# Kernel optimization log

Hardware: AMD Instinct MI355X
Metric: run time of the kernel (lower is better)

The kernel has to match this reference:

```python
import jax, jax.numpy as jnp
import numpy as np

G, N, F_IN, H, C = 128, 512, 128, 128, 10
LAMB = 1.0
NEG_SLOPE = 0.2
P_EDGE = 32.0 / N  # avg degree ~32


def setup_inputs() -> dict:
    key = jax.random.key(0)
    ks = jax.random.split(key, 12)
    x = jax.random.normal(ks[0], (G, N, F_IN), dtype=jnp.float32)
    # symmetric 0/1 adjacency without self loops (per-graph dense block)
    a = (jax.random.uniform(ks[1], (G, N, N)) < P_EDGE).astype(jnp.float32)
    adj = jnp.maximum(a, jnp.swapaxes(a, 1, 2)) * (1.0 - jnp.eye(N, dtype=jnp.float32))

    def lin(k, fi, fo):
        return (jax.random.normal(k, (fi, fo), dtype=jnp.float32) / np.float32(np.sqrt(fi)))

    return {
        "x": x, "adj": adj,
        "W1": lin(ks[2], F_IN, H), "b1": jnp.zeros((H,), jnp.float32),
        "W2": lin(ks[3], H, H), "b2": jnp.zeros((H,), jnp.float32),
        "W3": lin(ks[4], H, H), "b3": jnp.zeros((H,), jnp.float32),
        "att1_s": 0.1 * jax.random.normal(ks[5], (H,), dtype=jnp.float32),
        "att1_d": 0.1 * jax.random.normal(ks[6], (H,), dtype=jnp.float32),
        "att2_s": 0.1 * jax.random.normal(ks[7], (H,), dtype=jnp.float32),
        "att2_d": 0.1 * jax.random.normal(ks[8], (H,), dtype=jnp.float32),
        "Wl1": lin(ks[9], 2 * H, H), "bl1": jnp.zeros((H,), jnp.float32),
        "Wl2": lin(ks[10], H, H // 2), "bl2": jnp.zeros((H // 2,), jnp.float32),
        "Wl3": lin(ks[11], H // 2, C), "bl3": jnp.zeros((C,), jnp.float32),
    }


def gcn(x, adj, W, b):
    # GCNConv: D^{-1/2} (A + I) D^{-1/2} X W + b  (self-loop weight 1, edge weights in adj)
    deg = adj.sum(-1) + 1.0                              # [G, n]
    dinv = jax.lax.rsqrt(deg)
    xw = x @ W                                           # [G, n, H]
    agg = jnp.einsum('gij,gjf->gif', adj, dinv[..., None] * xw)
    return dinv[..., None] * agg + (dinv * dinv)[..., None] * xw + b


def info_score(x, adj):
    # HGP-SL node information score: row-wise L1 norm of (I - D^{-1} A) X
    deg = jnp.maximum(adj.sum(-1), 1.0)
    agg = jnp.einsum('gij,gjf->gif', adj, x) / deg[..., None]
    return jnp.sum(jnp.abs(x - agg), axis=-1)            # [G, n]


def hgpsl_pool(x, adj, att_s, att_d, k):
    # top-k node selection by information score, then structure learning:
    # dense (sample=False) path: e_ij = leaky_relu(att.[x_i||x_j]) + lamb*A_ij, softmax over j
    s = info_score(x, adj)
    _, idx = jax.lax.top_k(s, k)                         # [G, k]
    xk = jnp.take_along_axis(x, idx[..., None], axis=1)  # [G, k, H]
    g = jnp.arange(x.shape[0])[:, None, None]
    ak = adj[g, idx[:, :, None], idx[:, None, :]]        # induced adjacency [G, k, k]
    e = jax.nn.leaky_relu((xk @ att_s)[:, :, None] + (xk @ att_d)[:, None, :], NEG_SLOPE)
    attn = jax.nn.softmax(e + LAMB * ak, axis=-1)        # new learned edge weights
    return xk, attn


def readout(x):
    # gmp || gap over nodes
    return jnp.concatenate([x.max(axis=1), x.mean(axis=1)], axis=-1)


def reference(x, adj, W1, b1, W2, b2, W3, b3, att1_s, att1_d, att2_s, att2_d,
              Wl1, bl1, Wl2, bl2, Wl3, bl3):
    h = jax.nn.relu(gcn(x, adj, W1, b1))
    h, a1 = hgpsl_pool(h, adj, att1_s, att1_d, N // 2)
    x1 = readout(h)
    h = jax.nn.relu(gcn(h, a1, W2, b2))
    h, a2 = hgpsl_pool(h, a1, att2_s, att2_d, N // 4)
    x2 = readout(h)
    h = jax.nn.relu(gcn(h, a2, W3, b3))
    x3 = readout(h)
    z = jax.nn.relu(x1) + jax.nn.relu(x2) + jax.nn.relu(x3)
    z = jax.nn.relu(z @ Wl1 + bl1)
    z = jax.nn.relu(z @ Wl2 + bl2)
    return jax.nn.softmax(z @ Wl3 + bl3, axis=-1)
```

## Files before the change

### kernel.cpp

```cpp
#include <hip/hip_runtime.h>

#define Gg   128
#define N1   512
#define FH   128
#define K1   256
#define K2   128

typedef unsigned short ush;
typedef __bf16 bf16x8 __attribute__((ext_vector_type(8)));
typedef float  floatx4 __attribute__((ext_vector_type(4)));

__device__ inline float wredsum(float v) {
#pragma unroll
    for (int o = 32; o; o >>= 1) v += __shfl_xor(v, o, 64);
    return v;
}
__device__ inline float wredmax(float v) {
#pragma unroll
    for (int o = 32; o; o >>= 1) v = fmaxf(v, __shfl_xor(v, o, 64));
    return v;
}
__device__ inline ush bf_rne(float x) {
    unsigned u = __float_as_uint(x);
    return (ush)((u + 0x7fffu + ((u >> 16) & 1u)) >> 16);
}
__device__ inline float bf2f(ush u) { return __uint_as_float((unsigned)u << 16); }
__device__ inline void split3(float v, ush& h, ush& m, ush& l) {
    h = bf_rne(v);
    float r1 = v - bf2f(h);
    m = bf_rne(r1);
    l = bf_rne(r1 - bf2f(m));
}
__device__ __forceinline__ bf16x8 expand_bits(unsigned word, int quad) {
    unsigned byte = (word >> (quad * 8)) & 0xffu;
    unsigned au[4] __attribute__((aligned(16)));
    au[0] = ((byte & 1u)   ? 0x3F80u : 0u) | ((byte & 2u)   ? 0x3F800000u : 0u);
    au[1] = ((byte & 4u)   ? 0x3F80u : 0u) | ((byte & 8u)   ? 0x3F800000u : 0u);
    au[2] = ((byte & 16u)  ? 0x3F80u : 0u) | ((byte & 32u)  ? 0x3F800000u : 0u);
    au[3] = ((byte & 64u)  ? 0x3F80u : 0u) | ((byte & 128u) ? 0x3F800000u : 0u);
    return *(const bf16x8*)au;
}

__global__ __launch_bounds__(256) void k_prep(const float* __restrict__ adj,
        float* __restrict__ dinv_gcn, float* __restrict__ dinv_info,
        unsigned* __restrict__ adjbits) {
    int wave = threadIdx.x >> 6, lane = threadIdx.x & 63;
    long long row = (long long)blockIdx.x * 4 + wave;
    const float* ar = adj + row * N1;
    float s = 0.f;
    unsigned myw = 0;
#pragma unroll
    for (int c = 0; c < 8; ++c) {
        float v = ar[c * 64 + lane];
        s += v;
        unsigned long long mk = __ballot(v != 0.0f);
        unsigned lo = (unsigned)mk, hi = (unsigned)(mk >> 32);
        if ((lane >> 1) == c) myw = (lane & 1) ? hi : lo;
    }
    if (lane < 16) adjbits[row * 16 + lane] = myw;
    s = wredsum(s);
    if (lane == 0) {
        dinv_gcn[row]  = rsqrtf(s + 1.0f);
        dinv_info[row] = 1.0f / fmaxf(s, 1.0f);
    }
}

__global__ __launch_bounds__(256) void k_gemm_rw(const float* __restrict__ A,
        const float* __restrict__ W, float* __restrict__ C,
        const float* __restrict__ rs) {
    __shared__ float Al[64][68];
    __shared__ float Wl[64][132];
    long long row0 = (long long)blockIdx.x * 64;
    int tid = threadIdx.x, tr = tid >> 4, tc = tid & 15;
    float acc[4][8] = {};
    for (int ch = 0; ch < 2; ++ch) {
        for (int p = tid; p < 1024; p += 256) {
            int r = p >> 4, c4 = p & 15;
            *(float4*)&Al[r][c4 * 4] = *(const float4*)(A + (row0 + r) * 128 + ch * 64 + c4 * 4);
        }
        for (int p = tid; p < 2048; p += 256) {
            int r = p >> 5, c4 = p & 31;
            *(float4*)&Wl[r][c4 * 4] = *(const float4*)(W + (ch * 64 + r) * 128 + c4 * 4);
        }
        __syncthreads();
        for (int k = 0; k < 64; ++k) {
            float4 w0 = *(const float4*)&Wl[k][tc * 8];
            float4 w1 = *(const float4*)&Wl[k][tc * 8 + 4];
            float w[8] = {w0.x, w0.y, w0.z, w0.w, w1.x, w1.y, w1.z, w1.w};
#pragma unroll
            for (int i = 0; i < 4; ++i) {
                float a = Al[tr * 4 + i][k];
#pragma unroll
                for (int j = 0; j < 8; ++j) acc[i][j] = fmaf(a, w[j], acc[i][j]);
            }
        }
        __syncthreads();
    }
#pragma unroll
    for (int i = 0; i < 4; ++i) {
        long long r = row0 + tr * 4 + i;
        float sc = rs ? rs[r] : 1.0f;
        *(float4*)(C + r * 128 + tc * 8)     = make_float4(sc * acc[i][0], sc * acc[i][1], sc * acc[i][2], sc * acc[i][3]);
        *(float4*)(C + r * 128 + tc * 8 + 4) = make_float4(sc * acc[i][4], sc * acc[i][5], sc * acc[i][6], sc * acc[i][7]);
    }
}

template<int KD>
__global__ __launch_bounds__(256) void k_tsplit(const float* __restrict__ feat,
        ush* __restrict__ Thi, ush* __restrict__ Tmid, ush* __restrict__ Tlo) {
    __shared__ float tile[64 * 65];
    int b = blockIdx.x;
    int cb = b & 1;
    long long row0 = (long long)(b >> 1) * 64;
    int g = (int)(row0 / KD);
    int rk0 = (int)(row0 % KD);
    int t = threadIdx.x;
    {
        int r0 = t >> 4, c4 = t & 15;
#pragma unroll
        for (int i = 0; i < 4; ++i) {
            int r = r0 + i * 16;
            float4 v = *(const float4*)(feat + (row0 + r) * 128 + cb * 64 + c4 * 4);
            tile[r * 65 + c4 * 4 + 0] = v.x;
            tile[r * 65 + c4 * 4 + 1] = v.y;
            tile[r * 65 + c4 * 4 + 2] = v.z;
            tile[r * 65 + c4 * 4 + 3] = v.w;
        }
    }
    __syncthreads();
    int tf = t >> 2, chunk = t & 3;
    ush hbuf[16] __attribute__((aligned(16)));
    ush mbuf[16] __attribute__((aligned(16)));
    ush lbuf[16] __attribute__((aligned(16)));
#pragma unroll
    for (int i = 0; i < 16; ++i) {
        int m = chunk * 16 + i;
        split3(tile[m * 65 + tf], hbuf[i], mbuf[i], lbuf[i]);
    }
    long long obase = ((long long)g * 128 + cb * 64 + tf) * KD + rk0 + chunk * 16;
    *(uint4*)(Thi + obase)      = *(const uint4*)&hbuf[0];
    *(uint4*)(Thi + obase + 8)  = *(const uint4*)&hbuf[8];
    *(uint4*)(Tmid + obase)     = *(const uint4*)&mbuf[0];
    *(uint4*)(Tmid + obase + 8) = *(const uint4*)&mbuf[8];
    *(uint4*)(Tlo + obase)      = *(const uint4*)&lbuf[0];
    *(uint4*)(Tlo + obase + 8)  = *(const uint4*)&lbuf[8];
}

template<int EPI>
__global__ __launch_bounds__(256) void k_aggbT(const unsigned* __restrict__ adjbits,
        const ush* __restrict__ Ahi, const ush* __restrict__ Amid, const ush* __restrict__ Alo,
        const float* __restrict__ dvec, const float* __restrict__ hx,
        const float* __restrict__ bias, float* __restrict__ outH, float* __restrict__ outS) {
    __shared__ unsigned bitsL[128 * 17];
    __shared__ float sred[2][128];
    int b = blockIdx.x;
    int g  = (b & 7) + ((b >> 5) << 3);
    int ib = (b >> 3) & 3;
    int tid = threadIdx.x;
    int w = tid >> 6, lane = tid & 63;
    int wm = w >> 1, wn = w & 1;
    int ln = lane & 15, quad = lane >> 4;
    {
        int r = tid >> 1, w8 = (tid & 1) * 8;
        const unsigned* src = adjbits + ((long long)(g * 512 + ib * 128 + r)) * 16 + w8;
        uint4 v0 = *(const uint4*)src;
        uint4 v1 = *(const uint4*)(src + 4);
        unsigned* dst = &bitsL[r * 17 + w8];
        dst[0] = v0.x; dst[1] = v0.y; dst[2] = v0.z; dst[3] = v0.w;
        dst[4] = v1.x; dst[5] = v1.y; dst[6] = v1.z; dst[7] = v1.w;
    }
    __syncthreads();
    floatx4 acc[4][4];
#pragma unroll
    for (int i = 0; i < 4; ++i)
#pragma unroll
        for (int j = 0; j < 4; ++j) { floatx4 z = {0.f, 0.f, 0.f, 0.f}; acc[i][j] = z; }

    long long aoff[4];
#pragma unroll
    for (int tm = 0; tm < 4; ++tm)
        aoff[tm] = ((long long)g * 128 + wm * 64 + tm * 16 + ln) * 512 + quad * 8;
    int boffL[4];
#pragma unroll
    for (int tn = 0; tn < 4; ++tn)
        boffL[tn] = (wn * 64 + tn * 16 + ln) * 17;

#pragma unroll 2
    for (int kt = 0; kt < 16; ++kt) {
        int kk = kt * 32;
        bf16x8 ah[4], am[4], al[4];
#pragma unroll
        for (int tm = 0; tm < 4; ++tm) {
            ah[tm] = *(const bf16x8*)(Ahi  + aoff[tm] + kk);
            am[tm] = *(const bf16x8*)(Amid + aoff[tm] + kk);
            al[tm] = *(const bf16x8*)(Alo  + aoff[tm] + kk);
        }
#pragma unroll
        for (int tn = 0; tn < 4; ++tn) {
            bf16x8 bb = expand_bits(bitsL[boffL[tn] + kt], quad);
#pragma unroll
            for (int tm = 0; tm < 4; ++tm) {
                acc[tm][tn] = __builtin_amdgcn_mfma_f32_16x16x32_bf16(ah[tm], bb, acc[tm][tn], 0, 0, 0);
                acc[tm][tn] = __builtin_amdgcn_mfma_f32_16x16x32_bf16(am[tm], bb, acc[tm][tn], 0, 0, 0);
                acc[tm][tn] = __builtin_amdgcn_mfma_f32_16x16x32_bf16(al[tm], bb, acc[tm][tn], 0, 0, 0);
            }
        }
    }
    if (EPI == 0) {
#pragma unroll
        for (int tn = 0; tn < 4; ++tn) {
            long long grow = (long long)g * 512 + ib * 128 + wn * 64 + tn * 16 + ln;
            float di = dvec[grow];
#pragma unroll
            for (int tm = 0; tm < 4; ++tm) {
                int f0 = wm * 64 + tm * 16 + quad * 4;
                float4 hv = *(const float4*)(hx + grow * 128 + f0);
                float4 bv = *(const float4*)(bias + f0);
                float4 o;
                o.x = fmaxf(fmaf(di, acc[tm][tn][0] + hv.x, bv.x), 0.f);
                o.y = fmaxf(fmaf(di, acc[tm][tn][1] + hv.y, bv.y), 0.f);
                o.z = fmaxf(fmaf(di, acc[tm][tn][2] + hv.z, bv.z), 0.f);
                o.w = fmaxf(fmaf(di, acc[tm][tn][3] + hv.w, bv.w), 0.f);
                *(float4*)(outH + grow * 128 + f0) = o;
            }
        }
    } else {
#pragma unroll
        for (int tn = 0; tn < 4; ++tn) {
            int il = wn * 64 + tn * 16 + ln;
            long long grow = (long long)g * 512 + ib * 128 + il;
            float di = dvec[grow];
            float p = 0.f;
#pragma unroll
            for (int tm = 0; tm < 4; ++tm) {
                int f0 = wm * 64 + tm * 16 + quad * 4;
                float4 hv = *(const float4*)(hx + grow * 128 + f0);
                p += fabsf(hv.x - acc[tm][tn][0] * di) + fabsf(hv.y - acc[tm][tn][1] * di)
                   + fabsf(hv.z - acc[tm][tn][2] * di) + fabsf(hv.w - acc[tm][tn][3] * di);
            }
            p += __shfl_xor(p, 16); p += __shfl_xor(p, 32);
            if (quad == 0) sred[wm][il] = p;
        }
        __syncthreads();
        if (tid < 128)
            outS[(long long)g * 512 + ib * 128 + tid] = sred[0][tid] + sred[1][tid];
    }
}

template<int KD, int TM, int EPI>
__global__ __launch_bounds__(256) void k_aggsT(
        const ush* __restrict__ Fhi, const ush* __restrict__ Fmid, const ush* __restrict__ Flo,
        const ush* __restrict__ Phi, const ush* __restrict__ Pmid, const ush* __restrict__ Plo,
        const float* __restrict__ dvec, const float* __restrict__ hx,
        const float* __restrict__ bias, float* __restrict__ outH, float* __restrict__ outS) {
    __shared__ float sred[2][128];
    constexpr int FB = TM * 32;
    constexpr int bpgF = 128 / FB;
    constexpr int bpgI = KD / 128;
    constexpr int BPG = bpgF * bpgI;
    int b = blockIdx.x;
    int g   = (b & 7) + ((b / (8 * BPG)) << 3);
    int sub = (b >> 3) % BPG;
    int fb = sub / bpgI, ib2 = sub % bpgI;
    int tid = threadIdx.x;
    int w = tid >> 6, lane = tid & 63;
    int wm = w >> 1, wn = w & 1;
    int ln = lane & 15, quad = lane >> 4;
    floatx4 acc[TM][4];
#pragma unroll
    for (int i = 0; i < TM; ++i)
#pragma unroll
        for (int j = 0; j < 4; ++j) { floatx4 z = {0.f, 0.f, 0.f, 0.f}; acc[i][j] = z; }

    long long aoff[TM], boff[4];
#pragma unroll
    for (int tm = 0; tm < TM; ++tm)
        aoff[tm] = ((long long)g * 128 + fb * FB + wm * (FB / 2) + tm * 16 + ln) * KD + quad * 8;
#pragma unroll
    for (int tn = 0; tn < 4; ++tn)
        boff[tn] = ((long long)g * KD + ib2 * 128 + wn * 64 + tn * 16 + ln) * KD + quad * 8;

#pragma unroll 2
    for (int kt = 0; kt < KD / 32; ++kt) {
        int kk = kt * 32;
        bf16x8 ah[TM], am[TM], al[TM];
#pragma unroll
        for (int tm = 0; tm < TM; ++tm) {
            ah[tm] = *(const bf16x8*)(Fhi  + aoff[tm] + kk);
            am[tm] = *(const bf16x8*)(Fmid + aoff[tm] + kk);
            al[tm] = *(const bf16x8*)(Flo  + aoff[tm] + kk);
        }
#pragma unroll
        for (int tn = 0; tn < 4; ++tn) {
            bf16x8 bh = *(const bf16x8*)(Phi  + boff[tn] + kk);
            bf16x8 bm = *(const bf16x8*)(Pmid + boff[tn] + kk);
            bf16x8 bl = *(const bf16x8*)(Plo  + boff[tn] + kk);
#pragma unroll
            for (int tm = 0; tm < TM; ++tm) {
                floatx4 a = acc[tm][tn];
                a = __builtin_amdgcn_mfma_f32_16x16x32_bf16(ah[tm], bh, a, 0, 0, 0);
                a = __builtin_amdgcn_mfma_f32_16x16x32_bf16(ah[tm], bm, a, 0, 0, 0);
                a = __builtin_amdgcn_mfma_f32_16x16x32_bf16(am[tm], bh, a, 0, 0, 0);
                a = __builtin_amdgcn_mfma_f32_16x16x32_bf16(ah[tm], bl, a, 0, 0, 0);
                a = __builtin_amdgcn_mfma_f32_16x16x32_bf16(al[tm], bh, a, 0, 0, 0);
                a = __builtin_amdgcn_mfma_f32_16x16x32_bf16(am[tm], bm, a, 0, 0, 0);
                acc[tm][tn] = a;
            }
        }
    }
    if (EPI == 0) {
#pragma unroll
        for (int tn = 0; tn < 4; ++tn) {
            long long grow = (long long)g * KD + ib2 * 128 + wn * 64 + tn * 16 + ln;
            float di = dvec[grow];
#pragma unroll
            for (int tm = 0; tm < TM; ++tm) {
                int f0 = fb * FB + wm * (FB / 2) + tm * 16 + quad * 4;
                float4 hv = *(const float4*)(hx + grow * 128 + f0);
                float4 bv = *(const float4*)(bias + f0);
                float4 o;
                o.x = fmaxf(fmaf(di, acc[tm][tn][0] + hv.x, bv.x), 0.f);
                o.y = fmaxf(fmaf(di, acc[tm][tn][1] + hv.y, bv.y), 0.f);
                o.z = fmaxf(fmaf(di, acc[tm][tn][2] + hv.z, bv.z), 0.f);
                o.w = fmaxf(fmaf(di, acc[tm][tn][3] + hv.w, bv.w), 0.f);
                *(float4*)(outH + grow * 128 + f0) = o;
            }
        }
    } else {
#pragma unroll
        for (int tn = 0; tn < 4; ++tn) {
            int il = wn * 64 + tn * 16 + ln;
            long long grow = (long long)g * KD + ib2 * 128 + il;
            float di = dvec[grow];
            float p = 0.f;
#pragma unroll
            for (int tm = 0; tm < TM; ++tm) {
                int f0 = fb * FB + wm * (FB / 2) + tm * 16 + quad * 4;
                float4 hv = *(const float4*)(hx + grow * 128 + f0);
                p += fabsf(hv.x - acc[tm][tn][0] * di) + fabsf(hv.y - acc[tm][tn][1] * di)
                   + fabsf(hv.z - acc[tm][tn][2] * di) + fabsf(hv.w - acc[tm][tn][3] * di);
            }
            p += __shfl_xor(p, 16); p += __shfl_xor(p, 32);
            if (quad == 0) sred[wm][il] = p;
        }
        __syncthreads();
        if (tid < 128)
            outS[(long long)g * KD + ib2 * 128 + tid] = sred[0][tid] + sred[1][tid];
    }
}

template<int NT, int KSEL>
__global__ __launch_bounds__(256) void k_topk(const float* __restrict__ s, int* __restrict__ idx) {
    __shared__ unsigned long long keys[NT];
    int g = blockIdx.x;
    const float* sg = s + g * NT;
    for (int t = threadIdx.x; t < NT; t += 256) {
        unsigned int b = __float_as_uint(sg[t]);
        unsigned int ord = (b & 0x80000000u) ? ~b : (b | 0x80000000u);
        keys[t] = ((unsigned long long)(~ord) << 32) | (unsigned int)t;
    }
    __syncthreads();
    for (int k = 2; k <= NT; k <<= 1) {
        for (int j = k >> 1; j > 0; j >>= 1) {
            for (int i = threadIdx.x; i < NT; i += 256) {
                int l = i ^ j;
                if (l > i) {
                    bool dir = ((i & k) == 0);
                    unsigned long long a = keys[i], b2 = keys[l];
                    bool sw = dir ? (a > b2) : (a < b2);
                    if (sw) { keys[i] = b2; keys[l] = a; }
                }
            }
            __syncthreads();
        }
    }
    for (int t = threadIdx.x; t < KSEL; t += 256)
        idx[g * KSEL + t] = (int)(keys[t] & 0xffffffffu);
}

template<int KK>
__global__ __launch_bounds__(256) void k_gather(const float* __restrict__ h, int srcN,
        const int* __restrict__ idx, const float* __restrict__ atts, const float* __restrict__ attd,
        float* __restrict__ xk, float* __restrict__ as_, float* __restrict__ ad_) {
    int wave = threadIdx.x >> 6, lane = threadIdx.x & 63;
    int r = blockIdx.x * 4 + wave;
    int g = r / KK;
    int j = idx[r];
    float2 v = *(const float2*)(h + ((long long)g * srcN + j) * 128 + lane * 2);
    *(float2*)(xk + (long long)r * 128 + lane * 2) = v;
    float2 sv = *(const float2*)(atts + lane * 2);
    float2 dv = *(const float2*)(attd + lane * 2);
    float ps = v.x * sv.x + v.y * sv.y;
    float pd = v.x * dv.x + v.y * dv.y;
    ps = wredsum(ps); pd = wredsum(pd);
    if (lane == 0) { as_[r] = ps; ad_[r] = pd; }
}

__global__ __launch_bounds__(256) void k_attn1b(const unsigned* __restrict__ adjbits,
        const int* __restrict__ idx, const float* __restrict__ as_, const float* __restrict__ ad_,
        float* __restrict__ a1, ush* __restrict__ Ahi, ush* __restrict__ Amid, ush* __restrict__ Alo,
        float* __restrict__ dgo, float* __restrict__ dio) {
    __shared__ int   idxL[K1];
    __shared__ float adL[K1];
    __shared__ unsigned bitsW[4][20];
    __shared__ float rowL[4][K1];
    int g = blockIdx.x / (K1 / 4);
    int wave = threadIdx.x >> 6, lane = threadIdx.x & 63;
    int i = (blockIdx.x % (K1 / 4)) * 4 + wave;
    for (int t = threadIdx.x; t < K1; t += 256) { idxL[t] = idx[g * K1 + t]; adL[t] = ad_[g * K1 + t]; }
    __syncthreads();
    int ri = idxL[i];
    if (lane < 4) {
        uint4 v = *(const uint4*)(adjbits + ((long long)(g * 512 + ri)) * 16 + lane * 4);
        bitsW[wave][lane * 4 + 0] = v.x; bitsW[wave][lane * 4 + 1] = v.y;
        bitsW[wave][lane * 4 + 2] = v.z; bitsW[wave][lane * 4 + 3] = v.w;
    }
    __syncthreads();
    float asi = as_[g * K1 + i];
    float vals[4];
    float m = -1e30f;
#pragma unroll
    for (int e = 0; e < 4; ++e) {
        int j = e * 64 + lane;
        float x = asi + adL[j];
        x = (x >= 0.f) ? x : 0.2f * x;
        int jj = idxL[j];
        unsigned bit = (bitsW[wave][jj >> 5] >> (jj & 31)) & 1u;
        x += (float)bit;
        vals[e] = x; m = fmaxf(m, x);
    }
    m = wredmax(m);
    float S = 0.f;
#pragma unroll
    for (int e = 0; e < 4; ++e) { vals[e] = expf(vals[e] - m); S += vals[e]; }
    S = wredsum(S);
    float inv = 1.f / S, rs = 0.f;
    float* orow = a1 + ((long long)g * K1 + i) * K1;
#pragma unroll
    for (int e = 0; e < 4; ++e) {
        float p = vals[e] * inv; rs += p;
        orow[e * 64 + lane] = p;
        rowL[wave][e * 64 + lane] = p;
    }
    rs = wredsum(rs);
    if (lane == 0) { dgo[g * K1 + i] = rsqrtf(rs + 1.f); dio[g * K1 + i] = 1.f / fmaxf(rs, 1.f); }
    long long sb = ((long long)g * K1 + i) * K1 + lane * 4;
    ush hb[4], mb[4], lb[4];
#pragma unroll
    for (int q = 0; q < 4; ++q) split3(rowL[wave][lane * 4 + q], hb[q], mb[q], lb[q]);
    *(ushort4*)(Ahi  + sb) = make_ushort4(hb[0], hb[1], hb[2], hb[3]);
    *(ushort4*)(Amid + sb) = make_ushort4(mb[0], mb[1], mb[2], mb[3]);
    *(ushort4*)(Alo  + sb) = make_ushort4(lb[0], lb[1], lb[2], lb[3]);
}

__global__ __launch_bounds__(256) void k_attn2(const float* __restrict__ a1,
        const int* __restrict__ idx, const float* __restrict__ as_, const float* __restrict__ ad_,
        ush* __restrict__ Ahi, ush* __restrict__ Amid, ush* __restrict__ Alo,
        float* __restrict__ dgo) {
    __shared__ int   idxL[K2];
    __shared__ float adL[K2];
    __shared__ float rowL[4][K1];
    int g = blockIdx.x / (K2 / 4);
    int wave = threadIdx.x >> 6, lane = threadIdx.x & 63;
    int i = (blockIdx.x % (K2 / 4)) * 4 + wave;
    for (int t = threadIdx.x; t < K2; t += 256) { idxL[t] = idx[g * K2 + t]; adL[t] = ad_[g * K2 + t]; }
    __syncthreads();
    int ri = idxL[i];
    const float* arow = a1 + ((long long)g * K1 + ri) * K1;
    for (int c = lane; c < K1; c += 64) rowL[wave][c] = arow[c];
    float asi = as_[g * K2 + i];
    float vals[2];
    float m = -1e30f;
#pragma unroll
    for (int e = 0; e < 2; ++e) {
        int j = e * 64 + lane;
        float x = asi + adL[j];
        x = (x >= 0.f) ? x : 0.2f * x;
        x += rowL[wave][idxL[j]];
        vals[e] = x; m = fmaxf(m, x);
    }
    m = wredmax(m);
    float S = 0.f;
#pragma unroll
    for (int e = 0; e < 2; ++e) { vals[e] = expf(vals[e] - m); S += vals[e]; }
    S = wredsum(S);
    float inv = 1.f / S, rs = 0.f;
#pragma unroll
    for (int e = 0; e < 2; ++e) {
        float p = vals[e] * inv; rs += p;
        rowL[wave][e * 64 + lane] = p;
    }
    rs = wredsum(rs);
    if (lane == 0) dgo[g * K2 + i] = rsqrtf(rs + 1.f);
    long long sb = ((long long)g * K2 + i) * K2 + lane * 2;
    ush hb[2], mb[2], lb[2];
#pragma unroll
    for (int q = 0; q < 2; ++q) split3(rowL[wave][lane * 2 + q], hb[q], mb[q], lb[q]);
    *(ushort2*)(Ahi  + sb) = make_ushort2(hb[0], hb[1]);
    *(ushort2*)(Amid + sb) = make_ushort2(mb[0], mb[1]);
    *(ushort2*)(Alo  + sb) = make_ushort2(lb[0], lb[1]);
}

template<int KK>
__global__ __launch_bounds__(128) void k_readout(const float* __restrict__ xk, float* __restrict__ xo) {
    int g = blockIdx.x, f = threadIdx.x;
    const float* p = xk + (long long)g * KK * 128 + f;
    float m = -1e30f, s = 0.f;
    for (int r = 0; r < KK; ++r) { float v = p[r * 128]; m = fmaxf(m, v); s += v; }
    xo[g * 256 + f] = m;
    xo[g * 256 + 128 + f] = s * (1.0f / KK);
}

__global__ __launch_bounds__(128) void k_mlp(const float* __restrict__ x1, const float* __restrict__ x2,
        const float* __restrict__ x3,
        const float* __restrict__ Wl1, const float* __restrict__ bl1,
        const float* __restrict__ Wl2, const float* __restrict__ bl2,
        const float* __restrict__ Wl3, const float* __restrict__ bl3,
        float* __restrict__ out) {
    __shared__ float z[256], z1[128], z2[64], lg[10];
    int g = blockIdx.x, t = threadIdx.x;
    for (int k = t; k < 256; k += 128)
        z[k] = fmaxf(x1[g * 256 + k], 0.f) + fmaxf(x2[g * 256 + k], 0.f) + fmaxf(x3[g * 256 + k], 0.f);
    __syncthreads();
    {
        float acc = bl1[t];
        for (int k = 0; k < 256; ++k) acc = fmaf(z[k], Wl1[k * 128 + t], acc);
        z1[t] = fmaxf(acc, 0.f);
    }
    __syncthreads();
    if (t < 64) {
        float acc = bl2[t];
        for (int k = 0; k < 128; ++k) acc = fmaf(z1[k], Wl2[k * 64 + t], acc);
        z2[t] = fmaxf(acc, 0.f);
    }
    __syncthreads();
    if (t < 10) {
        float acc = bl3[t];
        for (int k = 0; k < 64; ++k) acc = fmaf(z2[k], Wl3[k * 10 + t], acc);
        lg[t] = acc;
    }
    __syncthreads();
    if (t == 0) {
        float m = -1e30f;
        for (int c = 0; c < 10; ++c) m = fmaxf(m, lg[c]);
        float S = 0.f;
        float e[10];
        for (int c = 0; c < 10; ++c) { e[c] = expf(lg[c] - m); S += e[c]; }
        float inv = 1.f / S;
        for (int c = 0; c < 10; ++c) out[g * 10 + c] = e[c] * inv;
    }
}

extern "C" void kernel_launch(void* const* d_in, const int* in_sizes, int n_in,
                              void* d_out, int out_size, void* d_ws, size_t ws_size,
                              hipStream_t stream) {
    const float* x     = (const float*)d_in[0];
    const float* adj   = (const float*)d_in[1];
    const float* W1    = (const float*)d_in[2];
    const float* b1    = (const float*)d_in[3];
    const float* W2    = (const float*)d_in[4];
    const float* b2    = (const float*)d_in[5];
    const float* W3    = (const float*)d_in[6];
    const float* b3    = (const float*)d_in[7];
    const float* att1s = (const float*)d_in[8];
    const float* att1d = (const float*)d_in[9];
    const float* att2s = (const float*)d_in[10];
    const float* att2d = (const float*)d_in[11];
    const float* Wl1   = (const float*)d_in[12];
    const float* bl1   = (const float*)d_in[13];
    const float* Wl2   = (const float*)d_in[14];
    const float* bl2   = (const float*)d_in[15];
    const float* Wl3   = (const float*)d_in[16];
    const float* bl3   = (const float*)d_in[17];
    float* out = (float*)d_out;

    char* ws = (char*)d_ws;
    unsigned* adjbits = (unsigned*)(ws + 0);
    ush*   T1hi   = (ush*)  (ws + 4194304);
    ush*   T1mid  = (ush*)  (ws + 20971520);
    ush*   T1lo   = (ush*)  (ws + 37748736);
    ush*   T2hi   = (ush*)  (ws + 54525952);
    ush*   T2mid  = (ush*)  (ws + 71303168);
    ush*   T2lo   = (ush*)  (ws + 88080384);
    float* dxw1   = (float*)(ws + 104857600);
    float* h1     = dxw1;
    float* a1     = (float*)(ws + 138412032);
    ush*   A1hi   = (ush*)  (ws + 171966464);
    ush*   A1mid  = (ush*)  (ws + 188743680);
    ush*   A1lo   = (ush*)  (ws + 205520896);
    float* xk1    = (float*)(ws + 222298112);
    float* dxw2   = (float*)(ws + 239075328);
    ush*   Y2hi   = (ush*)  (ws + 255852544);
    ush*   Y2mid  = (ush*)  (ws + 264241152);
    ush*   Y2lo   = (ush*)  (ws + 272629760);
    float* h2     = (float*)(ws + 281018368);
    ush*   H2hi   = (ush*)  (ws + 297795584);
    ush*   H2mid  = (ush*)  (ws + 306184192);
    ush*   H2lo   = (ush*)  (ws + 314572800);
    float* xk2    = (float*)(ws + 322961408);
    ush*   A2hi   = (ush*)  (ws + 331350016);
    ush*   A2mid  = (ush*)  (ws + 335544320);
    ush*   A2lo   = (ush*)  (ws + 339738624);
    float* dxw3   = (float*)(ws + 343932928);
    ush*   Y3hi   = (ush*)  (ws + 352321536);
    ush*   Y3mid  = (ush*)  (ws + 356515840);
    ush*   Y3lo   = (ush*)  (ws + 360710144);
    float* h3     = (float*)(ws + 364904448);
    float* s1     = (float*)(ws + 373293056);
    int*   idx1   = (int*)  (ws + 373555200);
    float* as1    = (float*)(ws + 373817344);
    float* ad1    = (float*)(ws + 373948416);
    float* dinv_g1= (float*)(ws + 374079488);
    float* dinv_i1= (float*)(ws + 374341632);
    float* dinv_g2= (float*)(ws + 374603776);
    float* dinv_i2= (float*)(ws + 374734848);
    float* x1r    = (float*)(ws + 374865920);
    float* s2     = (float*)(ws + 374996992);
    int*   idx2   = (int*)  (ws + 375128064);
    float* as2    = (float*)(ws + 375193600);
    float* ad2    = (float*)(ws + 375259136);
    float* dinv_g3= (float*)(ws + 375324672);
    float* x2r    = (float*)(ws + 375390208);
    float* x3r    = (float*)(ws + 375521280);

    k_prep<<<Gg * N1 / 4, 256, 0, stream>>>(adj, dinv_g1, dinv_i1, adjbits);
    k_gemm_rw<<<Gg * N1 / 64, 256, 0, stream>>>(x, W1, dxw1, dinv_g1);
    k_tsplit<N1><<<Gg * 16, 256, 0, stream>>>(dxw1, T1hi, T1mid, T1lo);
    k_aggbT<0><<<512, 256, 0, stream>>>(adjbits, T1hi, T1mid, T1lo, dinv_g1, dxw1, b1, h1, nullptr);
    k_tsplit<N1><<<Gg * 16, 256, 0, stream>>>(h1, T2hi, T2mid, T2lo);
    k_aggbT<1><<<512, 256, 0, stream>>>(adjbits, T2hi, T2mid, T2lo, dinv_i1, h1, nullptr, nullptr, s1);
    k_topk<N1, K1><<<Gg, 256, 0, stream>>>(s1, idx1);
    k_gather<K1><<<Gg * K1 / 4, 256, 0, stream>>>(h1, N1, idx1, att1s, att1d, xk1, as1, ad1);
    k_readout<K1><<<Gg, 128, 0, stream>>>(xk1, x1r);
    k_attn1b<<<Gg * K1 / 4, 256, 0, stream>>>(adjbits, idx1, as1, ad1, a1, A1hi, A1mid, A1lo,
                                              dinv_g2, dinv_i2);

    k_gemm_rw<<<Gg * K1 / 64, 256, 0, stream>>>(xk1, W2, dxw2, dinv_g2);
    k_tsplit<K1><<<Gg * 8, 256, 0, stream>>>(dxw2, Y2hi, Y2mid, Y2lo);
    k_aggsT<K1, 4, 0><<<Gg * 2, 256, 0, stream>>>(Y2hi, Y2mid, Y2lo, A1hi, A1mid, A1lo,
                                                  dinv_g2, dxw2, b2, h2, nullptr);
    k_tsplit<K1><<<Gg * 8, 256, 0, stream>>>(h2, H2hi, H2mid, H2lo);
    k_aggsT<K1, 4, 1><<<Gg * 2, 256, 0, stream>>>(H2hi, H2mid, H2lo, A1hi, A1mid, A1lo,
                                                  dinv_i2, h2, nullptr, nullptr, s2);
    k_topk<K1, K2><<<Gg, 256, 0, stream>>>(s2, idx2);
    k_gather<K2><<<Gg * K2 / 4, 256, 0, stream>>>(h2, K1, idx2, att2s, att2d, xk2, as2, ad2);
    k_readout<K2><<<Gg, 128, 0, stream>>>(xk2, x2r);
    k_attn2<<<Gg * K2 / 4, 256, 0, stream>>>(a1, idx2, as2, ad2, A2hi, A2mid, A2lo, dinv_g3);

    k_gemm_rw<<<Gg * K2 / 64, 256, 0, stream>>>(xk2, W3, dxw3, dinv_g3);
    k_tsplit<K2><<<Gg * 4, 256, 0, stream>>>(dxw3, Y3hi, Y3mid, Y3lo);
    k_aggsT<K2, 2, 0><<<Gg * 2, 256, 0, stream>>>(Y3hi, Y3mid, Y3lo, A2hi, A2mid, A2lo,
                                                  dinv_g3, dxw3, b3, h3, nullptr);
    k_readout<K2><<<Gg, 128, 0, stream>>>(h3, x3r);

    k_mlp<<<Gg, 128, 0, stream>>>(x1r, x2r, x3r, Wl1, bl1, Wl2, bl2, Wl3, bl3, out);
}
```

Measured before the change: 652.0 us.

## Fuse hi/mid/lo split into GEMM epilogue and split aggregation over feature halves

The bf16 three-way split (transpose plus hi/mid/lo) now happens in the epilogue of the dense X·W GEMM, staged through shared memory. This removes three separate k_tsplit launches and their global round-trip. The bitmask and sparse aggregation kernels now split the 128 features into two 64-wide halves, doubling the grid and halving per-block accumulators to raise occupancy and parallelism. The info-score outputs therefore become atomicAdd accumulations, which needs memsets of s1/s2 beforehand and adds extra adjacency-bit and operand reloads per block.

```diff
diff --git a/kernel.cpp b/kernel.cpp
--- a/kernel.cpp
+++ b/kernel.cpp
@@ -65,43 +65,67 @@
     }
 }
 
-__global__ __launch_bounds__(256) void k_gemm_rw(const float* __restrict__ A,
+template<int KD>
+__global__ __launch_bounds__(256) void k_gemm_rwt(const float* __restrict__ A,
         const float* __restrict__ W, float* __restrict__ C,
-        const float* __restrict__ rs) {
-    __shared__ float Al[64][68];
-    __shared__ float Wl[64][132];
+        const float* __restrict__ rs,
+        ush* __restrict__ Thi, ush* __restrict__ Tmid, ush* __restrict__ Tlo) {
+    __shared__ float Al[64 * 68];
+    __shared__ float Wl[64 * 132];
     long long row0 = (long long)blockIdx.x * 64;
     int tid = threadIdx.x, tr = tid >> 4, tc = tid & 15;
     float acc[4][8] = {};
     for (int ch = 0; ch < 2; ++ch) {
         for (int p = tid; p < 1024; p += 256) {
             int r = p >> 4, c4 = p & 15;
-            *(float4*)&Al[r][c4 * 4] = *(const float4*)(A + (row0 + r) * 128 + ch * 64 + c4 * 4);
+            *(float4*)&Al[r * 68 + c4 * 4] = *(const float4*)(A + (row0 + r) * 128 + ch * 64 + c4 * 4);
         }
         for (int p = tid; p < 2048; p += 256) {
             int r = p >> 5, c4 = p & 31;
-            *(float4*)&Wl[r][c4 * 4] = *(const float4*)(W + (ch * 64 + r) * 128 + c4 * 4);
+            *(float4*)&Wl[r * 132 + c4 * 4] = *(const float4*)(W + (ch * 64 + r) * 128 + c4 * 4);
         }
         __syncthreads();
         for (int k = 0; k < 64; ++k) {
-            float4 w0 = *(const float4*)&Wl[k][tc * 8];
-            float4 w1 = *(const float4*)&Wl[k][tc * 8 + 4];
+            float4 w0 = *(const float4*)&Wl[k * 132 + tc * 8];
+            float4 w1 = *(const float4*)&Wl[k * 132 + tc * 8 + 4];
             float w[8] = {w0.x, w0.y, w0.z, w0.w, w1.x, w1.y, w1.z, w1.w};
 #pragma unroll
             for (int i = 0; i < 4; ++i) {
-                float a = Al[tr * 4 + i][k];
+                float a = Al[(tr * 4 + i) * 68 + k];
 #pragma unroll
                 for (int j = 0; j < 8; ++j) acc[i][j] = fmaf(a, w[j], acc[i][j]);
             }
         }
         __syncthreads();
     }
+    float* Cl = Wl;
 #pragma unroll
     for (int i = 0; i < 4; ++i) {
         long long r = row0 + tr * 4 + i;
         float sc = rs ? rs[r] : 1.0f;
-        *(float4*)(C + r * 128 + tc * 8)     = make_float4(sc * acc[i][0], sc * acc[i][1], sc * acc[i][2], sc * acc[i][3]);
-        *(float4*)(C + r * 128 + tc * 8 + 4) = make_float4(sc * acc[i][4], sc * acc[i][5], sc * acc[i][6], sc * acc[i][7]);
+        float v[8];
+#pragma unroll
+        for (int j = 0; j < 8; ++j) v[j] = sc * acc[i][j];
+        *(float4*)(C + r * 128 + tc * 8)     = make_float4(v[0], v[1], v[2], v[3]);
+        *(float4*)(C + r * 128 + tc * 8 + 4) = make_float4(v[4], v[5], v[6], v[7]);
+#pragma unroll
+        for (int j = 0; j < 8; ++j) Cl[(tr * 4 + i) * 129 + tc * 8 + j] = v[j];
+    }
+    __syncthreads();
+    int f = tid >> 1, half = tid & 1;
+    int g = (int)(row0 / KD), rk0 = (int)(row0 % KD);
+    ush hb[32] __attribute__((aligned(16)));
+    ush mb[32] __attribute__((aligned(16)));
+    ush lb[32] __attribute__((aligned(16)));
+#pragma unroll
+    for (int i = 0; i < 32; ++i)
+        split3(Cl[(half * 32 + i) * 129 + f], hb[i], mb[i], lb[i]);
+    long long ob = ((long long)g * 128 + f) * KD + rk0 + half * 32;
+#pragma unroll
+    for (int q = 0; q < 4; ++q) {
+        *(uint4*)(Thi  + ob + q * 8) = *(const uint4*)&hb[q * 8];
+        *(uint4*)(Tmid + ob + q * 8) = *(const uint4*)&mb[q * 8];
+        *(uint4*)(Tlo  + ob + q * 8) = *(const uint4*)&lb[q * 8];
     }
 }
 
@@ -154,8 +178,9 @@
     __shared__ unsigned bitsL[128 * 17];
     __shared__ float sred[2][128];
     int b = blockIdx.x;
-    int g  = (b & 7) + ((b >> 5) << 3);
-    int ib = (b >> 3) & 3;
+    int g  = (b & 7) + ((b >> 6) << 3);
+    int sub = (b >> 3) & 7;
+    int ib = sub & 3, fb = sub >> 2;
     int tid = threadIdx.x;
     int w = tid >> 6, lane = tid & 63;
     int wm = w >> 1, wn = w & 1;
@@ -170,16 +195,16 @@
         dst[4] = v1.x; dst[5] = v1.y; dst[6] = v1.z; dst[7] = v1.w;
     }
     __syncthreads();
-    floatx4 acc[4][4];
-#pragma unroll
-    for (int i = 0; i < 4; ++i)
+    floatx4 acc[2][4];
+#pragma unroll
+    for (int i = 0; i < 2; ++i)
 #pragma unroll
         for (int j = 0; j < 4; ++j) { floatx4 z = {0.f, 0.f, 0.f, 0.f}; acc[i][j] = z; }
 
-    long long aoff[4];
-#pragma unroll
-    for (int tm = 0; tm < 4; ++tm)
-        aoff[tm] = ((long long)g * 128 + wm * 64 + tm * 16 + ln) * 512 + quad * 8;
+    long long aoff[2];
+#pragma unroll
+    for (int tm = 0; tm < 2; ++tm)
+        aoff[tm] = ((long long)g * 128 + fb * 64 + wm * 32 + tm * 16 + ln) * 512 + quad * 8;
     int boffL[4];
 #pragma unroll
     for (int tn = 0; tn < 4; ++tn)
@@ -188,9 +213,9 @@
 #pragma unroll 2
     for (int kt = 0; kt < 16; ++kt) {
         int kk = kt * 32;
-        bf16x8 ah[4], am[4], al[4];
-#pragma unroll
-        for (int tm = 0; tm < 4; ++tm) {
+        bf16x8 ah[2], am[2], al[2];
+#pragma unroll
+        for (int tm = 0; tm < 2; ++tm) {
             ah[tm] = *(const bf16x8*)(Ahi  + aoff[tm] + kk);
             am[tm] = *(const bf16x8*)(Amid + aoff[tm] + kk);
             al[tm] = *(const bf16x8*)(Alo  + aoff[tm] + kk);
@@ -199,7 +224,7 @@
         for (int tn = 0; tn < 4; ++tn) {
             bf16x8 bb = expand_bits(bitsL[boffL[tn] + kt], quad);
 #pragma unroll
-            for (int tm = 0; tm < 4; ++tm) {
+            for (int tm = 0; tm < 2; ++tm) {
                 acc[tm][tn] = __builtin_amdgcn_mfma_f32_16x16x32_bf16(ah[tm], bb, acc[tm][tn], 0, 0, 0);
                 acc[tm][tn] = __builtin_amdgcn_mfma_f32_16x16x32_bf16(am[tm], bb, acc[tm][tn], 0, 0, 0);
                 acc[tm][tn] = __builtin_amdgcn_mfma_f32_16x16x32_bf16(al[tm], bb, acc[tm][tn], 0, 0, 0);
@@ -212,8 +237,8 @@
             long long grow = (long long)g * 512 + ib * 128 + wn * 64 + tn * 16 + ln;
             float di = dvec[grow];
 #pragma unroll
-            for (int tm = 0; tm < 4; ++tm) {
-                int f0 = wm * 64 + tm * 16 + quad * 4;
+            for (int tm = 0; tm < 2; ++tm) {
+                int f0 = fb * 64 + wm * 32 + tm * 16 + quad * 4;
                 float4 hv = *(const float4*)(hx + grow * 128 + f0);
                 float4 bv = *(const float4*)(bias + f0);
                 float4 o;
@@ -232,8 +257,8 @@
             float di = dvec[grow];
             float p = 0.f;
 #pragma unroll
-            for (int tm = 0; tm < 4; ++tm) {
-                int f0 = wm * 64 + tm * 16 + quad * 4;
+            for (int tm = 0; tm < 2; ++tm) {
+                int f0 = fb * 64 + wm * 32 + tm * 16 + quad * 4;
                 float4 hv = *(const float4*)(hx + grow * 128 + f0);
                 p += fabsf(hv.x - acc[tm][tn][0] * di) + fabsf(hv.y - acc[tm][tn][1] * di)
                    + fabsf(hv.z - acc[tm][tn][2] * di) + fabsf(hv.w - acc[tm][tn][3] * di);
@@ -243,21 +268,19 @@
         }
         __syncthreads();
         if (tid < 128)
-            outS[(long long)g * 512 + ib * 128 + tid] = sred[0][tid] + sred[1][tid];
-    }
-}
-
-template<int KD, int TM, int EPI>
+            atomicAdd(&outS[(long long)g * 512 + ib * 128 + tid], sred[0][tid] + sred[1][tid]);
+    }
+}
+
+template<int KD, int EPI>
 __global__ __launch_bounds__(256) void k_aggsT(
         const ush* __restrict__ Fhi, const ush* __restrict__ Fmid, const ush* __restrict__ Flo,
         const ush* __restrict__ Phi, const ush* __restrict__ Pmid, const ush* __restrict__ Plo,
         const float* __restrict__ dvec, const float* __restrict__ hx,
         const float* __restrict__ bias, float* __restrict__ outH, float* __restrict__ outS) {
     __shared__ float sred[2][128];
-    constexpr int FB = TM * 32;
-    constexpr int bpgF = 128 / FB;
     constexpr int bpgI = KD / 128;
-    constexpr int BPG = bpgF * bpgI;
+    constexpr int BPG = 2 * bpgI;
     int b = blockIdx.x;
     int g   = (b & 7) + ((b / (8 * BPG)) << 3);
     int sub = (b >> 3) % BPG;
@@ -266,16 +289,16 @@
     int w = tid >> 6, lane = tid & 63;
     int wm = w >> 1, wn = w & 1;
     int ln = lane & 15, quad = lane >> 4;
-    floatx4 acc[TM][4];
-#pragma unroll
-    for (int i = 0; i < TM; ++i)
+    floatx4 acc[2][4];
+#pragma unroll
+    for (int i = 0; i < 2; ++i)
 #pragma unroll
         for (int j = 0; j < 4; ++j) { floatx4 z = {0.f, 0.f, 0.f, 0.f}; acc[i][j] = z; }
 
-    long long aoff[TM], boff[4];
-#pragma unroll
-    for (int tm = 0; tm < TM; ++tm)
-        aoff[tm] = ((long long)g * 128 + fb * FB + wm * (FB / 2) + tm * 16 + ln) * KD + quad * 8;
+    long long aoff[2], boff[4];
+#pragma unroll
+    for (int tm = 0; tm < 2; ++tm)
+        aoff[tm] = ((long long)g * 128 + fb * 64 + wm * 32 + tm * 16 + ln) * KD + quad * 8;
 #pragma unroll
     for (int tn = 0; tn < 4; ++tn)
         boff[tn] = ((long long)g * KD + ib2 * 128 + wn * 64 + tn * 16 + ln) * KD + quad * 8;
@@ -283,9 +306,9 @@
 #pragma unroll 2
     for (int kt = 0; kt < KD / 32; ++kt) {
         int kk = kt * 32;
-        bf16x8 ah[TM], am[TM], al[TM];
-#pragma unroll
-        for (int tm = 0; tm < TM; ++tm) {
+        bf16x8 ah[2], am[2], al[2];
+#pragma unroll
+        for (int tm = 0; tm < 2; ++tm) {
             ah[tm] = *(const bf16x8*)(Fhi  + aoff[tm] + kk);
             am[tm] = *(const bf16x8*)(Fmid + aoff[tm] + kk);
             al[tm] = *(const bf16x8*)(Flo  + aoff[tm] + kk);
@@ -296,7 +319,7 @@
             bf16x8 bm = *(const bf16x8*)(Pmid + boff[tn] + kk);
             bf16x8 bl = *(const bf16x8*)(Plo  + boff[tn] + kk);
 #pragma unroll
-            for (int tm = 0; tm < TM; ++tm) {
+            for (int tm = 0; tm < 2; ++tm) {
                 floatx4 a = acc[tm][tn];
                 a = __builtin_amdgcn_mfma_f32_16x16x32_bf16(ah[tm], bh, a, 0, 0, 0);
                 a = __builtin_amdgcn_mfma_f32_16x16x32_bf16(ah[tm], bm, a, 0, 0, 0);
@@ -314,8 +337,8 @@
             long long grow = (long long)g * KD + ib2 * 128 + wn * 64 + tn * 16 + ln;
             float di = dvec[grow];
 #pragma unroll
-            for (int tm = 0; tm < TM; ++tm) {
-                int f0 = fb * FB + wm * (FB / 2) + tm * 16 + quad * 4;
+            for (int tm = 0; tm < 2; ++tm) {
+                int f0 = fb * 64 + wm * 32 + tm * 16 + quad * 4;
                 float4 hv = *(const float4*)(hx + grow * 128 + f0);
                 float4 bv = *(const float4*)(bias + f0);
                 float4 o;
@@ -334,8 +357,8 @@
             float di = dvec[grow];
             float p = 0.f;
 #pragma unroll
-            for (int tm = 0; tm < TM; ++tm) {
-                int f0 = fb * FB + wm * (FB / 2) + tm * 16 + quad * 4;
+            for (int tm = 0; tm < 2; ++tm) {
+                int f0 = fb * 64 + wm * 32 + tm * 16 + quad * 4;
                 float4 hv = *(const float4*)(hx + grow * 128 + f0);
                 p += fabsf(hv.x - acc[tm][tn][0] * di) + fabsf(hv.y - acc[tm][tn][1] * di)
                    + fabsf(hv.z - acc[tm][tn][2] * di) + fabsf(hv.w - acc[tm][tn][3] * di);
@@ -345,7 +368,7 @@
         }
         __syncthreads();
         if (tid < 128)
-            outS[(long long)g * KD + ib2 * 128 + tid] = sred[0][tid] + sred[1][tid];
+            atomicAdd(&outS[(long long)g * KD + ib2 * 128 + tid], sred[0][tid] + sred[1][tid]);
     }
 }
 
@@ -623,34 +646,34 @@
     float* x2r    = (float*)(ws + 375390208);
     float* x3r    = (float*)(ws + 375521280);
 
+    hipMemsetAsync(s1, 0, Gg * N1 * sizeof(float), stream);
+    hipMemsetAsync(s2, 0, Gg * K1 * sizeof(float), stream);
+
     k_prep<<<Gg * N1 / 4, 256, 0, stream>>>(adj, dinv_g1, dinv_i1, adjbits);
-    k_gemm_rw<<<Gg * N1 / 64, 256, 0, stream>>>(x, W1, dxw1, dinv_g1);
-    k_tsplit<N1><<<Gg * 16, 256, 0, stream>>>(dxw1, T1hi, T1mid, T1lo);
-    k_aggbT<0><<<512, 256, 0, stream>>>(adjbits, T1hi, T1mid, T1lo, dinv_g1, dxw1, b1, h1, nullptr);
+    k_gemm_rwt<N1><<<Gg * N1 / 64, 256, 0, stream>>>(x, W1, dxw1, dinv_g1, T1hi, T1mid, T1lo);
+    k_aggbT<0><<<1024, 256, 0, stream>>>(adjbits, T1hi, T1mid, T1lo, dinv_g1, dxw1, b1, h1, nullptr);
     k_tsplit<N1><<<Gg * 16, 256, 0, stream>>>(h1, T2hi, T2mid, T2lo);
-    k_aggbT<1><<<512, 256, 0, stream>>>(adjbits, T2hi, T2mid, T2lo, dinv_i1, h1, nullptr, nullptr, s1);
+    k_aggbT<1><<<1024, 256, 0, stream>>>(adjbits, T2hi, T2mid, T2lo, dinv_i1, h1, nullptr, nullptr, s1);
     k_topk<N1, K1><<<Gg, 256, 0, stream>>>(s1, idx1);
     k_gather<K1><<<Gg * K1 / 4, 256, 0, stream>>>(h1, N1, idx1, att1s, att1d, xk1, as1, ad1);
     k_readout<K1><<<Gg, 128, 0, stream>>>(xk1, x1r);
     k_attn1b<<<Gg * K1 / 4, 256, 0, stream>>>(adjbits, idx1, as1, ad1, a1, A1hi, A1mid, A1lo,
                                               dinv_g2, dinv_i2);
 
-    k_gemm_rw<<<Gg * K1 / 64, 256, 0, stream>>>(xk1, W2, dxw2, dinv_g2);
-    k_tsplit<K1><<<Gg * 8, 256, 0, stream>>>(dxw2, Y2hi, Y2mid, Y2lo);
-    k_aggsT<K1, 4, 0><<<Gg * 2, 256, 0, stream>>>(Y2hi, Y2mid, Y2lo, A1hi, A1mid, A1lo,
-                                                  dinv_g2, dxw2, b2, h2, nullptr);
+    k_gemm_rwt<K1><<<Gg * K1 / 64, 256, 0, stream>>>(xk1, W2, dxw2, dinv_g2, Y2hi, Y2mid, Y2lo);
+    k_aggsT<K1, 0><<<Gg * 4, 256, 0, stream>>>(Y2hi, Y2mid, Y2lo, A1hi, A1mid, A1lo,
+                                               dinv_g2, dxw2, b2, h2, nullptr);
     k_tsplit<K1><<<Gg * 8, 256, 0, stream>>>(h2, H2hi, H2mid, H2lo);
-    k_aggsT<K1, 4, 1><<<Gg * 2, 256, 0, stream>>>(H2hi, H2mid, H2lo, A1hi, A1mid, A1lo,
-                                                  dinv_i2, h2, nullptr, nullptr, s2);
+    k_aggsT<K1, 1><<<Gg * 4, 256, 0, stream>>>(H2hi, H2mid, H2lo, A1hi, A1mid, A1lo,
+                                               dinv_i2, h2, nullptr, nullptr, s2);
     k_topk<K1, K2><<<Gg, 256, 0, stream>>>(s2, idx2);
     k_gather<K2><<<Gg * K2 / 4, 256, 0, stream>>>(h2, K1, idx2, att2s, att2d, xk2, as2, ad2);
     k_readout<K2><<<Gg, 128, 0, stream>>>(xk2, x2r);
     k_attn2<<<Gg * K2 / 4, 256, 0, stream>>>(a1, idx2, as2, ad2, A2hi, A2mid, A2lo, dinv_g3);
 
-    k_gemm_rw<<<Gg * K2 / 64, 256, 0, stream>>>(xk2, W3, dxw3, dinv_g3);
-    k_tsplit<K2><<<Gg * 4, 256, 0, stream>>>(dxw3, Y3hi, Y3mid, Y3lo);
-    k_aggsT<K2, 2, 0><<<Gg * 2, 256, 0, stream>>>(Y3hi, Y3mid, Y3lo, A2hi, A2mid, A2lo,
-                                                  dinv_g3, dxw3, b3, h3, nullptr);
+    k_gemm_rwt<K2><<<Gg * K2 / 64, 256, 0, stream>>>(xk2, W3, dxw3, dinv_g3, Y3hi, Y3mid, Y3lo);
+    k_aggsT<K2, 0><<<Gg * 2, 256, 0, stream>>>(Y3hi, Y3mid, Y3lo, A2hi, A2mid, A2lo,
+                                               dinv_g3, dxw3, b3, h3, nullptr);
     k_readout<K2><<<Gg, 128, 0, stream>>>(h3, x3r);
 
     k_mlp<<<Gg, 128, 0, stream>>>(x1r, x2r, x3r, Wl1, bl1, Wl2, bl2, Wl3, bl3, out);
```

Measured after the change: 656.9 us. About the same (+0.8%).
